# Optimization experiments

Hardware: AMD Instinct MI355X
Metric: run time of the kernel (lower is better)

The kernel has to match this reference:

```python
import jax, jax.numpy as jnp
import numpy as np

N, D, H, L, E, G, C = 50000, 128, 128, 5, 800000, 512, 10


def setup_inputs() -> dict:
    key = jax.random.key(0)
    ks = jax.random.split(key, 16)
    s = 0.1  # normal init std (Weight_Initializer == 3 style; any init is fine for a math baseline)
    return {
        "x": jax.random.normal(ks[0], (N, D), jnp.float32),
        "edge_index": jax.random.randint(ks[1], (2, E), 0, N, jnp.int32),
        "edge_mask": jax.random.uniform(ks[2], (E,), jnp.float32),
        "batch": jnp.sort(jax.random.randint(ks[3], (N,), 0, G, jnp.int32)),
        "num_graphs": G,
        "eps": jnp.zeros((L,), jnp.float32),
        # per-GIN-layer 2-layer MLP (num_slp_layers=2): D -> H -> D, weights stored [in, out]
        "mlp_w1": jax.random.normal(ks[4], (L, D, H), jnp.float32) * s,
        "mlp_b1": jnp.zeros((L, H), jnp.float32),
        "mlp_w2": jax.random.normal(ks[5], (L, H, D), jnp.float32) * s,
        "mlp_b2": jnp.zeros((L, D), jnp.float32),
        # classifier head: lin1 [(L+1)*D -> (L+1)*D], lin2 [(L+1)*D -> C]
        "lin1_w": jax.random.normal(ks[6], ((L + 1) * D, (L + 1) * D), jnp.float32) * s,
        "lin1_b": jnp.zeros(((L + 1) * D,), jnp.float32),
        "lin2_w": jax.random.normal(ks[7], ((L + 1) * D, C), jnp.float32) * s,
        "lin2_b": jnp.zeros((C,), jnp.float32),
    }


def reference(x, edge_index, edge_mask, batch, num_graphs, eps,
              mlp_w1, mlp_b1, mlp_w2, mlp_b2, lin1_w, lin1_b, lin2_w, lin2_b):
    n = x.shape[0]
    src, dst = edge_index[0], edge_index[1]
    embeds = [x]
    h = x
    for l in range(eps.shape[0]):
        # A @ h with A[src,dst] = edge_mask: gather neighbor feats, weight, scatter-add to src
        agg = jax.ops.segment_sum(edge_mask[:, None] * h[dst], src, num_segments=n)  # [N,D]
        pooled = agg + (1.0 + eps[l]) * h
        h1 = jax.nn.relu(pooled @ mlp_w1[l] + mlp_b1[l])
        h = jax.nn.relu(h1 @ mlp_w2[l] + mlp_b2[l])
        embeds.append(h)
    stacked = jnp.stack(embeds)  # [L+1, N, D]
    # global_add_pool per layer, then per-graph concat across layers -> [G, (L+1)*D]
    pooled_g = jax.vmap(lambda e: jax.ops.segment_sum(e, batch, num_segments=num_graphs))(stacked)
    merged = jnp.transpose(pooled_g, (1, 0, 2)).reshape(num_graphs, -1)
    lin1_out = jax.nn.relu(merged @ lin1_w + lin1_b)  # dropout p=0 -> identity
    lin2_out = lin1_out @ lin2_w + lin2_b
    return jax.nn.softmax(lin2_out, axis=1)  # [G, C]
```

## Files before the change

kernel.cpp:

```cpp
#include <hip/hip_runtime.h>


typedef __bf16 bf16x8 __attribute__((ext_vector_type(8)));
typedef float f32x4 __attribute__((ext_vector_type(4)));

static inline int ceil_div(int a, int b) { return (a + b - 1) / b; }

__device__ inline ushort bf_rne(float v) {
  unsigned u = __float_as_uint(v);
  return (ushort)((u + 0x7fffu + ((u >> 16) & 1u)) >> 16);
}
__device__ inline float bf2f(ushort u) { return __uint_as_float((unsigned)u << 16); }
__device__ inline float bf2f_lo(unsigned g) { return __uint_as_float(g << 16); }
__device__ inline float bf2f_hi(unsigned g) { return __uint_as_float(g & 0xffff0000u); }

__global__ void k_hist(const int* __restrict__ src, int* __restrict__ deg, int E) {
  int i = blockIdx.x * blockDim.x + threadIdx.x;
  if (i < E) atomicAdd(&deg[src[i]], 1);
}

__global__ __launch_bounds__(256) void k_scan1(const int* __restrict__ deg,
                                               int* __restrict__ excl,
                                               int* __restrict__ bsum, int N) {
  __shared__ int tsum[256];
  int b = blockIdx.x, t = threadIdx.x;
  int base = b * 1024 + t * 4;
  int v0 = 0, v1 = 0, v2 = 0, v3 = 0;
  if (base + 3 < N) {
    int4 q = *(const int4*)&deg[base];
    v0 = q.x; v1 = q.y; v2 = q.z; v3 = q.w;
  } else {
    if (base + 0 < N) v0 = deg[base + 0];
    if (base + 1 < N) v1 = deg[base + 1];
    if (base + 2 < N) v2 = deg[base + 2];
    if (base + 3 < N) v3 = deg[base + 3];
  }
  tsum[t] = v0 + v1 + v2 + v3;
  __syncthreads();
  for (int off = 1; off < 256; off <<= 1) {
    int x = (t >= off) ? tsum[t - off] : 0;
    __syncthreads();
    tsum[t] += x;
    __syncthreads();
  }
  int pre = (t == 0) ? 0 : tsum[t - 1];
  if (base < N)     excl[base]     = pre;
  if (base + 1 < N) excl[base + 1] = pre + v0;
  if (base + 2 < N) excl[base + 2] = pre + v0 + v1;
  if (base + 3 < N) excl[base + 3] = pre + v0 + v1 + v2;
  if (t == 255) bsum[b] = tsum[255];
}

__global__ __launch_bounds__(256) void k_scan2(const int* __restrict__ bsum,
                                               int* __restrict__ boff, int nb,
                                               int* __restrict__ rowptr_last) {
  __shared__ int s[256];
  int t = threadIdx.x;
  s[t] = (t < nb) ? bsum[t] : 0;
  __syncthreads();
  for (int off = 1; off < 256; off <<= 1) {
    int x = (t >= off) ? s[t - off] : 0;
    __syncthreads();
    s[t] += x;
    __syncthreads();
  }
  if (t < nb) boff[t] = (t == 0) ? 0 : s[t - 1];
  if (t == 255) *rowptr_last = s[255];
}

__global__ __launch_bounds__(256) void k_scan3(const int* __restrict__ excl,
                                               const int* __restrict__ boff,
                                               int* __restrict__ rowptr,
                                               int* __restrict__ cursor, int N) {
  int i = blockIdx.x * 256 + threadIdx.x;
  if (i < N) {
    int v = excl[i] + boff[i >> 10];
    rowptr[i] = v;
    cursor[i] = v;
  }
}

__global__ void k_scatter(const int* __restrict__ src, const int* __restrict__ dst,
                          const float* __restrict__ mask, int* __restrict__ cursor,
                          int2* __restrict__ sedge, int E) {
  int i = blockIdx.x * blockDim.x + threadIdx.x;
  if (i < E) {
    int s = src[i];
    int p = atomicAdd(&cursor[s], 1);
    sedge[p] = make_int2(dst[i], __float_as_int(mask[i]));
  }
}

__global__ __launch_bounds__(256) void k_tobf16(const float* __restrict__ in,
                                                ushort* __restrict__ out, int n) {
  int base = (blockIdx.x * 256 + threadIdx.x) * 4;
  if (base + 3 < n) {
    float4 v = *(const float4*)&in[base];
    ushort4 o;
    o.x = bf_rne(v.x); o.y = bf_rne(v.y); o.z = bf_rne(v.z); o.w = bf_rne(v.w);
    *(ushort4*)&out[base] = o;
  } else {
    for (int k = base; k < n; ++k) out[k] = bf_rne(in[k]);
  }
}

__global__ __launch_bounds__(256) void k_prepw(const float* __restrict__ W,
                                               ushort* __restrict__ hi,
                                               ushort* __restrict__ lo,
                                               int K, int N) {
  __shared__ float t[32][33];
  int mat = blockIdx.z;
  const float* Wm = W + (size_t)mat * K * N;
  ushort* him = hi + (size_t)mat * K * N;
  ushort* lom = lo + (size_t)mat * K * N;
  int k0 = blockIdx.x * 32, n0 = blockIdx.y * 32;
  int tx = threadIdx.x & 31, ty = threadIdx.x >> 5;
#pragma unroll
  for (int r = 0; r < 32; r += 8)
    t[ty + r][tx] = Wm[(size_t)(k0 + ty + r) * N + n0 + tx];
  __syncthreads();
#pragma unroll
  for (int r = 0; r < 32; r += 8) {
    float v = t[tx][ty + r];
    size_t o = (size_t)(n0 + ty + r) * K + k0 + tx;
    ushort h = bf_rne(v);
    him[o] = h;
    lom[o] = bf_rne(v - bf2f(h));
  }
}

__global__ __launch_bounds__(128) void k_agg(const ushort* __restrict__ h,
                                             const int* __restrict__ rowptr,
                                             const int2* __restrict__ sedge,
                                             const float* __restrict__ eps, int layer,
                                             ushort* __restrict__ pooled, int N) {
  int v = blockIdx.x * 2 + (threadIdx.x >> 6);
  int lane = threadIdx.x & 63;
  if (v >= N) return;
  int beg = rowptr[v], end = rowptr[v + 1];
  float ax[8] = {}, ay[8] = {};
  int j = beg;
  for (; j + 8 <= end; j += 8) {
    int2 e[8];
    unsigned g[8];
#pragma unroll
    for (int q = 0; q < 8; ++q) e[q] = sedge[j + q];
#pragma unroll
    for (int q = 0; q < 8; ++q)
      g[q] = *(const unsigned*)&h[(size_t)e[q].x * 128 + lane * 2];
#pragma unroll
    for (int q = 0; q < 8; ++q) {
      float m = __int_as_float(e[q].y);
      ax[q] = fmaf(m, bf2f_lo(g[q]), ax[q]);
      ay[q] = fmaf(m, bf2f_hi(g[q]), ay[q]);
    }
  }
  for (; j + 2 <= end; j += 2) {
    int2 e0 = sedge[j], e1 = sedge[j + 1];
    unsigned g0 = *(const unsigned*)&h[(size_t)e0.x * 128 + lane * 2];
    unsigned g1 = *(const unsigned*)&h[(size_t)e1.x * 128 + lane * 2];
    ax[0] = fmaf(__int_as_float(e0.y), bf2f_lo(g0), ax[0]);
    ay[0] = fmaf(__int_as_float(e0.y), bf2f_hi(g0), ay[0]);
    ax[1] = fmaf(__int_as_float(e1.y), bf2f_lo(g1), ax[1]);
    ay[1] = fmaf(__int_as_float(e1.y), bf2f_hi(g1), ay[1]);
  }
  if (j < end) {
    int2 e = sedge[j];
    unsigned g = *(const unsigned*)&h[(size_t)e.x * 128 + lane * 2];
    float m = __int_as_float(e.y);
    ax[0] = fmaf(m, bf2f_lo(g), ax[0]);
    ay[0] = fmaf(m, bf2f_hi(g), ay[0]);
  }
  float sx = ((ax[0] + ax[1]) + (ax[2] + ax[3])) + ((ax[4] + ax[5]) + (ax[6] + ax[7]));
  float sy = ((ay[0] + ay[1]) + (ay[2] + ay[3])) + ((ay[4] + ay[5]) + (ay[6] + ay[7]));
  float ep = 1.0f + eps[layer];
  unsigned gs = *(const unsigned*)&h[(size_t)v * 128 + lane * 2];
  sx = fmaf(ep, bf2f_lo(gs), sx);
  sy = fmaf(ep, bf2f_hi(gs), sy);
  unsigned outw = (unsigned)bf_rne(sx) | ((unsigned)bf_rne(sy) << 16);
  *(unsigned*)&pooled[(size_t)v * 128 + lane * 2] = outw;
}

__global__ __launch_bounds__(256) void k_mlp(
    const ushort* __restrict__ pooled,
    const ushort* __restrict__ w1t, const float* __restrict__ b1,
    const ushort* __restrict__ w2t, const float* __restrict__ b2,
    ushort* __restrict__ hout, int N) {
  __shared__ ushort As[64][128];
  __shared__ ushort Ws[128][128];
  __shared__ ushort H1s[64][128];
  int tid = threadIdx.x;
  int w = tid >> 6, lane = tid & 63;
  int row0 = blockIdx.x * 64;
  int wr = w >> 1, wc = w & 1;

#pragma unroll
  for (int i = 0; i < 4; ++i) {
    int f = i * 256 + tid;
    int r = f >> 4, c8 = (f & 15) * 8;
    int ksw = c8 ^ ((r & 7) << 3);
    if (row0 + r < N) {
      *(bf16x8*)&As[r][ksw] = *(const bf16x8*)&pooled[(size_t)(row0 + r) * 128 + c8];
    } else {
      ushort4 z = {0, 0, 0, 0};
      *(ushort4*)&As[r][ksw] = z;
      *(ushort4*)&As[r][ksw + 4] = z;
    }
  }
#pragma unroll
  for (int i = 0; i < 8; ++i) {
    int f = i * 256 + tid;
    int r = f >> 4, c8 = (f & 15) * 8;
    *(bf16x8*)&Ws[r][c8 ^ ((r & 7) << 3)] = *(const bf16x8*)&w1t[(size_t)r * 128 + c8];
  }
  __syncthreads();

  f32x4 acc[2][4];
#pragma unroll
  for (int m = 0; m < 2; ++m)
#pragma unroll
    for (int n = 0; n < 4; ++n) acc[m][n] = (f32x4){0.f, 0.f, 0.f, 0.f};
#pragma unroll
  for (int ks = 0; ks < 4; ++ks) {
    int kk = ks * 32 + (lane >> 4) * 8;
    bf16x8 a[2], b[4];
#pragma unroll
    for (int m = 0; m < 2; ++m) {
      int r = wr * 32 + m * 16 + (lane & 15);
      a[m] = *(bf16x8*)&As[r][kk ^ ((r & 7) << 3)];
    }
#pragma unroll
    for (int n = 0; n < 4; ++n) {
      int r = wc * 64 + n * 16 + (lane & 15);
      b[n] = *(bf16x8*)&Ws[r][kk ^ ((r & 7) << 3)];
    }
#pragma unroll
    for (int m = 0; m < 2; ++m)
#pragma unroll
      for (int n = 0; n < 4; ++n)
        acc[m][n] = __builtin_amdgcn_mfma_f32_16x16x32_bf16(a[m], b[n], acc[m][n], 0, 0, 0);
  }
#pragma unroll
  for (int m = 0; m < 2; ++m) {
    int rbase = wr * 32 + m * 16 + (lane >> 4) * 4;
#pragma unroll
    for (int n = 0; n < 4; ++n) {
      int col = wc * 64 + n * 16 + (lane & 15);
      float bb = b1[col];
#pragma unroll
      for (int r = 0; r < 4; ++r) {
        int row = rbase + r;
        float v = fmaxf(acc[m][n][r] + bb, 0.f);
        H1s[row][col ^ ((row & 7) << 3)] = bf_rne(v);
      }
    }
  }
  __syncthreads();

#pragma unroll
  for (int i = 0; i < 8; ++i) {
    int f = i * 256 + tid;
    int r = f >> 4, c8 = (f & 15) * 8;
    *(bf16x8*)&Ws[r][c8 ^ ((r & 7) << 3)] = *(const bf16x8*)&w2t[(size_t)r * 128 + c8];
  }
  __syncthreads();

#pragma unroll
  for (int m = 0; m < 2; ++m)
#pragma unroll
    for (int n = 0; n < 4; ++n) acc[m][n] = (f32x4){0.f, 0.f, 0.f, 0.f};
#pragma unroll
  for (int ks = 0; ks < 4; ++ks) {
    int kk = ks * 32 + (lane >> 4) * 8;
    bf16x8 a[2], b[4];
#pragma unroll
    for (int m = 0; m < 2; ++m) {
      int r = wr * 32 + m * 16 + (lane & 15);
      a[m] = *(bf16x8*)&H1s[r][kk ^ ((r & 7) << 3)];
    }
#pragma unroll
    for (int n = 0; n < 4; ++n) {
      int r = wc * 64 + n * 16 + (lane & 15);
      b[n] = *(bf16x8*)&Ws[r][kk ^ ((r & 7) << 3)];
    }
#pragma unroll
    for (int m = 0; m < 2; ++m)
#pragma unroll
      for (int n = 0; n < 4; ++n)
        acc[m][n] = __builtin_amdgcn_mfma_f32_16x16x32_bf16(a[m], b[n], acc[m][n], 0, 0, 0);
  }
#pragma unroll
  for (int m = 0; m < 2; ++m) {
    int rbase = row0 + wr * 32 + m * 16 + (lane >> 4) * 4;
#pragma unroll
    for (int n = 0; n < 4; ++n) {
      int col = wc * 64 + n * 16 + (lane & 15);
      float bb = b2[col];
#pragma unroll
      for (int r = 0; r < 4; ++r) {
        int row = rbase + r;
        if (row < N) {
          float v = fmaxf(acc[m][n][r] + bb, 0.f);
          hout[(size_t)row * 128 + col] = bf_rne(v);
        }
      }
    }
  }
}

template <int RELU, int OUT_BF16, int SPLITW>
__global__ __launch_bounds__(256) void k_mgemm(const ushort* __restrict__ A,
                                               const ushort* __restrict__ Wt_hi,
                                               const ushort* __restrict__ Wt_lo,
                                               const float* __restrict__ bias,
                                               void* __restrict__ Cout,
                                               int M, int N, int K) {
  __shared__ ushort As[64][128];
  __shared__ ushort Ws_hi[64][128];
  __shared__ ushort Ws_lo[SPLITW ? 64 : 1][SPLITW ? 128 : 1];
  int tid = threadIdx.x;
  int row0 = blockIdx.y * 64, col0 = blockIdx.x * 64;
  int w = tid >> 6, lane = tid & 63;
  int wr = w >> 1, wc = w & 1;
  f32x4 acc[2][2] = {};
  int nk = K >> 7;
  for (int kc = 0; kc < nk; ++kc) {
    int k0 = kc << 7;
    if (kc) __syncthreads();
#pragma unroll
    for (int i = 0; i < 4; ++i) {
      int f = i * 256 + tid;
      int r = f >> 4, c8 = (f & 15) * 8;
      int ksw = c8 ^ ((r & 7) << 3);
      if (row0 + r < M) {
        *(bf16x8*)&As[r][ksw] = *(const bf16x8*)&A[(size_t)(row0 + r) * K + k0 + c8];
      } else {
        ushort4 z = {0, 0, 0, 0};
        *(ushort4*)&As[r][ksw] = z;
        *(ushort4*)&As[r][ksw + 4] = z;
      }
    }
#pragma unroll
    for (int i = 0; i < 4; ++i) {
      int f = i * 256 + tid;
      int r = f >> 4, c8 = (f & 15) * 8;
      int ksw = c8 ^ ((r & 7) << 3);
      *(bf16x8*)&Ws_hi[r][ksw] = *(const bf16x8*)&Wt_hi[(size_t)(col0 + r) * K + k0 + c8];
      if (SPLITW)
        *(bf16x8*)&Ws_lo[r][ksw] = *(const bf16x8*)&Wt_lo[(size_t)(col0 + r) * K + k0 + c8];
    }
    __syncthreads();
#pragma unroll
    for (int ks = 0; ks < 4; ++ks) {
      int kk = ks * 32 + (lane >> 4) * 8;
      bf16x8 a[2], bh[2], bl[2];
#pragma unroll
      for (int m = 0; m < 2; ++m) {
        int r = wr * 32 + m * 16 + (lane & 15);
        a[m] = *(bf16x8*)&As[r][kk ^ ((r & 7) << 3)];
      }
#pragma unroll
      for (int n = 0; n < 2; ++n) {
        int r = wc * 32 + n * 16 + (lane & 15);
        int ksw = kk ^ ((r & 7) << 3);
        bh[n] = *(bf16x8*)&Ws_hi[r][ksw];
        if (SPLITW) bl[n] = *(bf16x8*)&Ws_lo[r][ksw];
      }
#pragma unroll
      for (int m = 0; m < 2; ++m)
#pragma unroll
        for (int n = 0; n < 2; ++n) {
          acc[m][n] = __builtin_amdgcn_mfma_f32_16x16x32_bf16(a[m], bh[n], acc[m][n], 0, 0, 0);
          if (SPLITW)
            acc[m][n] = __builtin_amdgcn_mfma_f32_16x16x32_bf16(a[m], bl[n], acc[m][n], 0, 0, 0);
        }
    }
  }
#pragma unroll
  for (int m = 0; m < 2; ++m) {
    int rbase = row0 + wr * 32 + m * 16 + (lane >> 4) * 4;
#pragma unroll
    for (int n = 0; n < 2; ++n) {
      int col = col0 + wc * 32 + n * 16 + (lane & 15);
      float b = bias[col];
#pragma unroll
      for (int r = 0; r < 4; ++r) {
        int row = rbase + r;
        if (row < M) {
          float v = acc[m][n][r] + b;
          if (RELU) v = fmaxf(v, 0.f);
          if (OUT_BF16)
            ((ushort*)Cout)[(size_t)row * N + col] = bf_rne(v);
          else
            ((float*)Cout)[(size_t)row * N + col] = v;
        }
      }
    }
  }
}

__global__ __launch_bounds__(128) void k_pool_all(
    const ushort* __restrict__ f0, const ushort* __restrict__ f1,
    const ushort* __restrict__ f2, const ushort* __restrict__ f3,
    const ushort* __restrict__ f4, const ushort* __restrict__ f5,
    const int* __restrict__ batch, ushort* __restrict__ pg, int N, int L1) {
  __shared__ float red[2][64][2];
  int g = blockIdx.x;
  int slot = blockIdx.y;
  const ushort* feat;
  switch (slot) {
    case 0: feat = f0; break;
    case 1: feat = f1; break;
    case 2: feat = f2; break;
    case 3: feat = f3; break;
    case 4: feat = f4; break;
    default: feat = f5; break;
  }
  int w = threadIdx.x >> 6, lane = threadIdx.x & 63;
  int lo = 0, hi = N;
  while (lo < hi) {
    int mid = (lo + hi) >> 1;
    if (batch[mid] < g) lo = mid + 1; else hi = mid;
  }
  int s = lo;
  hi = N;
  while (lo < hi) {
    int mid = (lo + hi) >> 1;
    if (batch[mid] < g + 1) lo = mid + 1; else hi = mid;
  }
  int e = lo;
  float a0 = 0.f, a1 = 0.f;
#pragma unroll 4
  for (int v = s + w; v < e; v += 2) {
    unsigned u = *(const unsigned*)&feat[(size_t)v * 128 + lane * 2];
    a0 += bf2f_lo(u);
    a1 += bf2f_hi(u);
  }
  red[w][lane][0] = a0;
  red[w][lane][1] = a1;
  __syncthreads();
  if (w == 0) {
    a0 = red[0][lane][0] + red[1][lane][0];
    a1 = red[0][lane][1] + red[1][lane][1];
    unsigned outw = (unsigned)bf_rne(a0) | ((unsigned)bf_rne(a1) << 16);
    *(unsigned*)&pg[((size_t)g * L1 + slot) * 128 + lane * 2] = outw;
  }
}

__global__ __launch_bounds__(64) void k_lin2_softmax(const float* __restrict__ A,
                                                     const float* __restrict__ W,
                                                     const float* __restrict__ b,
                                                     float* __restrict__ out, int K, int C) {
  constexpr int CMAX = 16;
  int g = blockIdx.x;
  int lane = threadIdx.x;
  float acc[CMAX];
#pragma unroll
  for (int c = 0; c < CMAX; ++c) acc[c] = 0.f;
  for (int k = lane; k < K; k += 64) {
    float a = A[(size_t)g * K + k];
#pragma unroll
    for (int c = 0; c < CMAX; ++c)
      if (c < C) acc[c] = fmaf(a, W[(size_t)k * C + c], acc[c]);
  }
#pragma unroll
  for (int off = 32; off; off >>= 1)
#pragma unroll
    for (int c = 0; c < CMAX; ++c) acc[c] += __shfl_xor(acc[c], off, 64);
  if (lane == 0) {
    float mx = -3.0e38f;
#pragma unroll
    for (int c = 0; c < CMAX; ++c)
      if (c < C) {
        acc[c] += b[c];
        mx = fmaxf(mx, acc[c]);
      }
    float sum = 0.f;
#pragma unroll
    for (int c = 0; c < CMAX; ++c)
      if (c < C) {
        acc[c] = expf(acc[c] - mx);
        sum += acc[c];
      }
    float inv = 1.f / sum;
#pragma unroll
    for (int c = 0; c < CMAX; ++c)
      if (c < C) out[(size_t)g * C + c] = acc[c] * inv;
  }
}

extern "C" void kernel_launch(void* const* d_in, const int* in_sizes, int n_in,
                              void* d_out, int out_size, void* d_ws, size_t ws_size,
                              hipStream_t stream) {
  const float* x     = (const float*)d_in[0];
  const int*   eidx  = (const int*)d_in[1];
  const float* emask = (const float*)d_in[2];
  const int*   batch = (const int*)d_in[3];
  const float* eps   = (const float*)d_in[5];
  const float* w1    = (const float*)d_in[6];
  const float* b1    = (const float*)d_in[7];
  const float* w2    = (const float*)d_in[8];
  const float* b2    = (const float*)d_in[9];
  const float* l1w   = (const float*)d_in[10];
  const float* l1b   = (const float*)d_in[11];
  const float* l2w   = (const float*)d_in[12];
  const float* l2b   = (const float*)d_in[13];

  const int N = in_sizes[3];
  const int E = in_sizes[2];
  const int L = in_sizes[5];
  const int D = in_sizes[0] / N;
  const int C = in_sizes[13];
  const int G = out_size / C;
  const int L1 = L + 1;
  const int H = in_sizes[7] / L;
  const int F = L1 * D;

  const int* src = eidx;
  const int* dst = eidx + E;

  char* p = (char*)d_ws;
  auto carve = [&](size_t bytes) -> void* {
    void* r = (void*)p;
    p += (bytes + 255) & ~(size_t)255;
    return r;
  };
  int*    rowptr = (int*)carve((size_t)(N + 1) * 4);
  int*    cursor = (int*)carve((size_t)N * 4);
  int*    deg    = (int*)carve((size_t)N * 4);
  int*    excl   = (int*)carve((size_t)N * 4);
  int*    bsum   = (int*)carve(256 * 4);
  int*    boff   = (int*)carve(256 * 4);
  int2*   sedge  = (int2*)carve((size_t)E * 8);
  ushort* xb     = (ushort*)carve((size_t)N * D * 2);
  ushort* pooled = (ushort*)carve((size_t)N * D * 2);
  ushort* hb[5];
  for (int l = 0; l < 5; ++l) hb[l] = (ushort*)carve((size_t)N * D * 2);
  ushort* pg     = (ushort*)carve((size_t)G * F * 2);
  float*  l1out  = (float*)carve((size_t)G * F * 4);
  ushort* w1t_hi = (ushort*)carve((size_t)L * D * H * 2);
  ushort* w1t_lo = (ushort*)carve((size_t)L * D * H * 2);
  ushort* w2t_hi = (ushort*)carve((size_t)L * H * D * 2);
  ushort* w2t_lo = (ushort*)carve((size_t)L * H * D * 2);
  ushort* l1t_hi = (ushort*)carve((size_t)F * F * 2);
  ushort* l1t_lo = (ushort*)carve((size_t)F * F * 2);
  (void)ws_size;

  const int nb = ceil_div(N, 1024);
  hipMemsetAsync(deg, 0, (size_t)N * 4, stream);
  k_hist<<<ceil_div(E, 256), 256, 0, stream>>>(src, deg, E);
  k_scan1<<<nb, 256, 0, stream>>>(deg, excl, bsum, N);
  k_scan2<<<1, 256, 0, stream>>>(bsum, boff, nb, &rowptr[N]);
  k_scan3<<<ceil_div(N, 256), 256, 0, stream>>>(excl, boff, rowptr, cursor, N);
  k_scatter<<<ceil_div(E, 256), 256, 0, stream>>>(src, dst, emask, cursor, sedge, E);

  k_tobf16<<<ceil_div(N * D, 1024), 256, 0, stream>>>(x, xb, N * D);
  k_prepw<<<dim3(D / 32, H / 32, L), 256, 0, stream>>>(w1, w1t_hi, w1t_lo, D, H);
  k_prepw<<<dim3(H / 32, D / 32, L), 256, 0, stream>>>(w2, w2t_hi, w2t_lo, H, D);
  k_prepw<<<dim3(F / 32, F / 32, 1), 256, 0, stream>>>(l1w, l1t_hi, l1t_lo, F, F);

  const ushort* h_in = xb;
  for (int l = 0; l < L; ++l) {
    k_agg<<<ceil_div(N, 2), 128, 0, stream>>>(h_in, rowptr, sedge, eps, l, pooled, N);
    k_mlp<<<ceil_div(N, 64), 256, 0, stream>>>(
        pooled, w1t_hi + (size_t)l * D * H, b1 + (size_t)l * H,
        w2t_hi + (size_t)l * H * D, b2 + (size_t)l * D, hb[l], N);
    h_in = hb[l];
  }

  k_pool_all<<<dim3(G, L1), 128, 0, stream>>>(xb, hb[0], hb[1], hb[2], hb[3], hb[4],
                                              batch, pg, N, L1);

  k_mgemm<1, 0, 1><<<dim3(F / 64, ceil_div(G, 64)), 256, 0, stream>>>(
      pg, l1t_hi, l1t_lo, l1b, l1out, G, F, F);
  k_lin2_softmax<<<G, 64, 0, stream>>>(l1out, l2w, l2b, (float*)d_out, F, C);
}
```

Before: 428.5 us.

## Fuse scan kernels, merge MLP weight prep, unroll aggregation, read MLP A directly

Merges the scan2 and scan3 kernels, so every scan3 block redoes the small block-sum scan itself and one launch disappears. Replaces the two per-layer MLP weight-prep launches with one kernel that writes only the high bf16 part, since the low part was never used. Adds a 16-edge unrolled loop in the aggregation kernel to keep more gathers in flight. The MLP kernel now reads A fragments straight from global memory instead of staging them in LDS. That saves shared memory and a barrier stage, but the A loads are uncoalesced and repeat across the two column warps.

```diff
diff --git a/kernel.cpp b/kernel.cpp
--- a/kernel.cpp
+++ b/kernel.cpp
@@ -51,9 +51,10 @@
   if (t == 255) bsum[b] = tsum[255];
 }
 
-__global__ __launch_bounds__(256) void k_scan2(const int* __restrict__ bsum,
-                                               int* __restrict__ boff, int nb,
-                                               int* __restrict__ rowptr_last) {
+__global__ __launch_bounds__(256) void k_scan3(const int* __restrict__ excl,
+                                               const int* __restrict__ bsum, int nb,
+                                               int* __restrict__ rowptr,
+                                               int* __restrict__ cursor, int N) {
   __shared__ int s[256];
   int t = threadIdx.x;
   s[t] = (t < nb) ? bsum[t] : 0;
@@ -64,20 +65,15 @@
     s[t] += x;
     __syncthreads();
   }
-  if (t < nb) boff[t] = (t == 0) ? 0 : s[t - 1];
-  if (t == 255) *rowptr_last = s[255];
-}
-
-__global__ __launch_bounds__(256) void k_scan3(const int* __restrict__ excl,
-                                               const int* __restrict__ boff,
-                                               int* __restrict__ rowptr,
-                                               int* __restrict__ cursor, int N) {
-  int i = blockIdx.x * 256 + threadIdx.x;
+  int i = blockIdx.x * 256 + t;
   if (i < N) {
-    int v = excl[i] + boff[i >> 10];
+    int blk = i >> 10;
+    int boff = blk ? s[blk - 1] : 0;
+    int v = excl[i] + boff;
     rowptr[i] = v;
     cursor[i] = v;
   }
+  if (i == N - 1) rowptr[N] = s[nb - 1];
 }
 
 __global__ void k_scatter(const int* __restrict__ src, const int* __restrict__ dst,
@@ -104,28 +100,47 @@
   }
 }
 
+__global__ __launch_bounds__(256) void k_prepw12(const float* __restrict__ W1,
+                                                 const float* __restrict__ W2,
+                                                 ushort* __restrict__ hi1,
+                                                 ushort* __restrict__ hi2, int L) {
+  __shared__ float t[32][33];
+  int z = blockIdx.z;
+  const float* Wm = (z < L) ? (W1 + (size_t)z * 128 * 128)
+                            : (W2 + (size_t)(z - L) * 128 * 128);
+  ushort* him = (z < L) ? (hi1 + (size_t)z * 128 * 128)
+                        : (hi2 + (size_t)(z - L) * 128 * 128);
+  int k0 = blockIdx.x * 32, n0 = blockIdx.y * 32;
+  int tx = threadIdx.x & 31, ty = threadIdx.x >> 5;
+#pragma unroll
+  for (int r = 0; r < 32; r += 8)
+    t[ty + r][tx] = Wm[(size_t)(k0 + ty + r) * 128 + n0 + tx];
+  __syncthreads();
+#pragma unroll
+  for (int r = 0; r < 32; r += 8) {
+    float v = t[tx][ty + r];
+    him[(size_t)(n0 + ty + r) * 128 + k0 + tx] = bf_rne(v);
+  }
+}
+
 __global__ __launch_bounds__(256) void k_prepw(const float* __restrict__ W,
                                                ushort* __restrict__ hi,
                                                ushort* __restrict__ lo,
                                                int K, int N) {
   __shared__ float t[32][33];
-  int mat = blockIdx.z;
-  const float* Wm = W + (size_t)mat * K * N;
-  ushort* him = hi + (size_t)mat * K * N;
-  ushort* lom = lo + (size_t)mat * K * N;
   int k0 = blockIdx.x * 32, n0 = blockIdx.y * 32;
   int tx = threadIdx.x & 31, ty = threadIdx.x >> 5;
 #pragma unroll
   for (int r = 0; r < 32; r += 8)
-    t[ty + r][tx] = Wm[(size_t)(k0 + ty + r) * N + n0 + tx];
+    t[ty + r][tx] = W[(size_t)(k0 + ty + r) * N + n0 + tx];
   __syncthreads();
 #pragma unroll
   for (int r = 0; r < 32; r += 8) {
     float v = t[tx][ty + r];
     size_t o = (size_t)(n0 + ty + r) * K + k0 + tx;
     ushort h = bf_rne(v);
-    him[o] = h;
-    lom[o] = bf_rne(v - bf2f(h));
+    hi[o] = h;
+    lo[o] = bf_rne(v - bf2f(h));
   }
 }
 
@@ -140,6 +155,21 @@
   int beg = rowptr[v], end = rowptr[v + 1];
   float ax[8] = {}, ay[8] = {};
   int j = beg;
+  for (; j + 16 <= end; j += 16) {
+    int2 e[16];
+    unsigned g[16];
+#pragma unroll
+    for (int q = 0; q < 16; ++q) e[q] = sedge[j + q];
+#pragma unroll
+    for (int q = 0; q < 16; ++q)
+      g[q] = *(const unsigned*)&h[(size_t)e[q].x * 128 + lane * 2];
+#pragma unroll
+    for (int q = 0; q < 16; ++q) {
+      float m = __int_as_float(e[q].y);
+      ax[q & 7] = fmaf(m, bf2f_lo(g[q]), ax[q & 7]);
+      ay[q & 7] = fmaf(m, bf2f_hi(g[q]), ay[q & 7]);
+    }
+  }
   for (; j + 8 <= end; j += 8) {
     int2 e[8];
     unsigned g[8];
@@ -186,7 +216,6 @@
     const ushort* __restrict__ w1t, const float* __restrict__ b1,
     const ushort* __restrict__ w2t, const float* __restrict__ b2,
     ushort* __restrict__ hout, int N) {
-  __shared__ ushort As[64][128];
   __shared__ ushort Ws[128][128];
   __shared__ ushort H1s[64][128];
   int tid = threadIdx.x;
@@ -195,19 +224,6 @@
   int wr = w >> 1, wc = w & 1;
 
 #pragma unroll
-  for (int i = 0; i < 4; ++i) {
-    int f = i * 256 + tid;
-    int r = f >> 4, c8 = (f & 15) * 8;
-    int ksw = c8 ^ ((r & 7) << 3);
-    if (row0 + r < N) {
-      *(bf16x8*)&As[r][ksw] = *(const bf16x8*)&pooled[(size_t)(row0 + r) * 128 + c8];
-    } else {
-      ushort4 z = {0, 0, 0, 0};
-      *(ushort4*)&As[r][ksw] = z;
-      *(ushort4*)&As[r][ksw + 4] = z;
-    }
-  }
-#pragma unroll
   for (int i = 0; i < 8; ++i) {
     int f = i * 256 + tid;
     int r = f >> 4, c8 = (f & 15) * 8;
@@ -226,8 +242,9 @@
     bf16x8 a[2], b[4];
 #pragma unroll
     for (int m = 0; m < 2; ++m) {
-      int r = wr * 32 + m * 16 + (lane & 15);
-      a[m] = *(bf16x8*)&As[r][kk ^ ((r & 7) << 3)];
+      int arow = row0 + wr * 32 + m * 16 + (lane & 15);
+      if (arow >= N) arow = N - 1;
+      a[m] = *(const bf16x8*)&pooled[(size_t)arow * 128 + kk];
     }
 #pragma unroll
     for (int n = 0; n < 4; ++n) {
@@ -530,7 +547,6 @@
   int*    deg    = (int*)carve((size_t)N * 4);
   int*    excl   = (int*)carve((size_t)N * 4);
   int*    bsum   = (int*)carve(256 * 4);
-  int*    boff   = (int*)carve(256 * 4);
   int2*   sedge  = (int2*)carve((size_t)E * 8);
   ushort* xb     = (ushort*)carve((size_t)N * D * 2);
   ushort* pooled = (ushort*)carve((size_t)N * D * 2);
@@ -539,9 +555,7 @@
   ushort* pg     = (ushort*)carve((size_t)G * F * 2);
   float*  l1out  = (float*)carve((size_t)G * F * 4);
   ushort* w1t_hi = (ushort*)carve((size_t)L * D * H * 2);
-  ushort* w1t_lo = (ushort*)carve((size_t)L * D * H * 2);
   ushort* w2t_hi = (ushort*)carve((size_t)L * H * D * 2);
-  ushort* w2t_lo = (ushort*)carve((size_t)L * H * D * 2);
   ushort* l1t_hi = (ushort*)carve((size_t)F * F * 2);
   ushort* l1t_lo = (ushort*)carve((size_t)F * F * 2);
   (void)ws_size;
@@ -550,14 +564,12 @@
   hipMemsetAsync(deg, 0, (size_t)N * 4, stream);
   k_hist<<<ceil_div(E, 256), 256, 0, stream>>>(src, deg, E);
   k_scan1<<<nb, 256, 0, stream>>>(deg, excl, bsum, N);
-  k_scan2<<<1, 256, 0, stream>>>(bsum, boff, nb, &rowptr[N]);
-  k_scan3<<<ceil_div(N, 256), 256, 0, stream>>>(excl, boff, rowptr, cursor, N);
+  k_scan3<<<ceil_div(N, 256), 256, 0, stream>>>(excl, bsum, nb, rowptr, cursor, N);
   k_scatter<<<ceil_div(E, 256), 256, 0, stream>>>(src, dst, emask, cursor, sedge, E);
 
   k_tobf16<<<ceil_div(N * D, 1024), 256, 0, stream>>>(x, xb, N * D);
-  k_prepw<<<dim3(D / 32, H / 32, L), 256, 0, stream>>>(w1, w1t_hi, w1t_lo, D, H);
-  k_prepw<<<dim3(H / 32, D / 32, L), 256, 0, stream>>>(w2, w2t_hi, w2t_lo, H, D);
-  k_prepw<<<dim3(F / 32, F / 32, 1), 256, 0, stream>>>(l1w, l1t_hi, l1t_lo, F, F);
+  k_prepw12<<<dim3(4, 4, 2 * L), 256, 0, stream>>>(w1, w2, w1t_hi, w2t_hi, L);
+  k_prepw<<<dim3(F / 32, F / 32), 256, 0, stream>>>(l1w, l1t_hi, l1t_lo, F, F);
 
   const ushort* h_in = xb;
   for (int l = 0; l < L; ++l) {
```

Result: no change. 421.9 us (-1.5%).
